# Performance work log

Hardware: AMD Instinct MI355X
Metric: run time of the kernel (lower is better)

## Reference

```python
import jax, jax.numpy as jnp
import numpy as np

DELTA_HEADING = 15.0
DELTA_BEARING = 15.0
N_HEADING = int(360 // 15)  # 24
N_BEARING = int(360 // 15)  # 24
MASK_FILL = 1e24


def setup_inputs() -> dict:
    key = jax.random.key(0)
    k1, k2, k3, k4, k5, k6 = jax.random.split(key, 6)
    N, B, H = 128, 256, 128
    hidden_state = jax.random.normal(k1, (N, B, H), dtype=jnp.float32)
    # distances in a realistic positive range
    distance_matrix = jax.random.uniform(k2, (B, N, N), dtype=jnp.float32, minval=0.0, maxval=10.0)
    bearing_matrix = jax.random.uniform(k3, (B, N, N), dtype=jnp.float32, minval=0.0, maxval=360.0)
    heading_matrix = jax.random.uniform(k4, (B, N, N), dtype=jnp.float32, minval=0.0, maxval=360.0)
    # mostly-valid sequence mask (bool, per batch x vessel)
    sequence_mask = jax.random.uniform(k5, (B, N)) > 0.1
    domain = jax.random.normal(k6, (N_HEADING, N_BEARING), dtype=jnp.float32)
    return {
        "hidden_state": hidden_state,
        "distance_matrix": distance_matrix,
        "bearing_matrix": bearing_matrix,
        "heading_matrix": heading_matrix,
        "sequence_mask": sequence_mask,
        "domain": domain,
    }


def reference(hidden_state, distance_matrix, bearing_matrix, heading_matrix, sequence_mask, domain):
    # indices into learned domain table
    idx1 = jnp.clip(jnp.floor(heading_matrix / DELTA_HEADING), 0, N_HEADING - 1).astype(jnp.int32)
    idx2 = jnp.clip(jnp.floor(bearing_matrix / DELTA_BEARING), 0, N_BEARING - 1).astype(jnp.int32)
    # pairwise validity mask: (B,N,1) & (B,1,N)
    wmask = sequence_mask[:, :, None] & sequence_mask[:, None, :]
    dist = jnp.where(wmask, distance_matrix, MASK_FILL)
    weights = jax.nn.softplus(domain[idx1, idx2] - dist)  # (B,N,N)
    # hidden_state: (N,B,H) -> (B,N,H); weighted sum over neighbors j
    h = jnp.swapaxes(hidden_state, 0, 1)
    weighted_hidden = jnp.tanh(jnp.einsum('bij,bjh->bih', weights, h))
    weighted_hidden = jnp.where(sequence_mask[:, :, None], weighted_hidden, 0.0)
    return weighted_hidden
```

## Files before the change

kernel.cpp:

```cpp
#include <hip/hip_runtime.h>

#define NV 128
#define NB 256
#define NH 128
#define KC 32
#define HSTR 136

typedef __attribute__((ext_vector_type(8))) unsigned short ushort8;
typedef __attribute__((ext_vector_type(4))) float f32x4;
typedef __attribute__((ext_vector_type(8))) __bf16 bf16x8;

__device__ __forceinline__ unsigned short f2bf(float x) {
  unsigned u = __builtin_bit_cast(unsigned, x);
  return (unsigned short)((u + 0x7fffu + ((u >> 16) & 1u)) >> 16);
}
__device__ __forceinline__ float bf2f(unsigned short h) {
  return __builtin_bit_cast(float, (unsigned)h << 16);
}

__launch_bounds__(512, 1)
__global__ void spatial_attn_mfma(const float* __restrict__ hidden,
                                  const float* __restrict__ dist,
                                  const float* __restrict__ brg,
                                  const float* __restrict__ hdg,
                                  const unsigned char* __restrict__ maskraw,
                                  const float* __restrict__ domain,
                                  float* __restrict__ out) {
  __shared__ unsigned short thi[NH * HSTR];
  __shared__ unsigned short tlo[NH * HSTR];
  __shared__ float dom[24 * 24];
  __shared__ float maskf[NV];
  __shared__ int kindsh;

  const int tid = threadIdx.x;
  const int lane = tid & 63;
  const int wv = tid >> 6;
  const int b = blockIdx.x;

  for (int k = tid; k < 576; k += 512) dom[k] = domain[k];
  if (tid == 0) kindsh = 1;
  const unsigned char s1 = maskraw[(size_t)(b & 63) * 512 + 4 * (tid & 127) + 1];
  __syncthreads();
  if (s1 != 0) kindsh = 0;
  __syncthreads();
  if (tid < NV) {
    const int m = kindsh ? ((const int*)maskraw)[b * NV + tid]
                         : (int)maskraw[b * NV + tid];
    maskf[tid] = (m != 0) ? 1.0f : 0.0f;
  }

  {
    const int shh = tid & 127;
    const int sj = (tid >> 7) * 32;
#pragma unroll
    for (int g = 0; g < 2; ++g) {
      const int jb = sj + g * 16;
      float v[16];
#pragma unroll
      for (int k = 0; k < 16; ++k)
        v[k] = hidden[((size_t)(jb + k) * NB + b) * NH + shh];
      ushort8 ph0, ph1, pl0, pl1;
#pragma unroll
      for (int k = 0; k < 8; ++k) {
        const unsigned short h = f2bf(v[k]);
        ph0[k] = h;
        pl0[k] = f2bf(v[k] - bf2f(h));
      }
#pragma unroll
      for (int k = 0; k < 8; ++k) {
        const unsigned short h = f2bf(v[8 + k]);
        ph1[k] = h;
        pl1[k] = f2bf(v[8 + k] - bf2f(h));
      }
      *(ushort8*)&thi[shh * HSTR + jb] = ph0;
      *(ushort8*)&thi[shh * HSTR + jb + 8] = ph1;
      *(ushort8*)&tlo[shh * HSTR + jb] = pl0;
      *(ushort8*)&tlo[shh * HSTR + jb + 8] = pl1;
    }
  }

  const int fm = lane & 15;
  const int j0 = (lane >> 4) * 8;
  const int arow = 16 * wv + fm;

  const float* dR = dist + ((size_t)b * NV + arow) * NV;
  const float* bR = brg + ((size_t)b * NV + arow) * NV;
  const float* gR = hdg + ((size_t)b * NV + arow) * NV;

  float4 pd0 = *(const float4*)&dR[j0];
  float4 pd1 = *(const float4*)&dR[j0 + 4];
  float4 pb0 = *(const float4*)&bR[j0];
  float4 pb1 = *(const float4*)&bR[j0 + 4];
  float4 pg0 = *(const float4*)&gR[j0];
  float4 pg1 = *(const float4*)&gR[j0 + 4];

  f32x4 acc[8];
#pragma unroll
  for (int t = 0; t < 8; ++t) acc[t] = (f32x4)0.0f;

  __syncthreads();

#pragma unroll
  for (int cs = 0; cs < 4; ++cs) {
    const int jc = cs * KC;

    const float dv[8] = {pd0.x, pd0.y, pd0.z, pd0.w, pd1.x, pd1.y, pd1.z, pd1.w};
    const float bv[8] = {pb0.x, pb0.y, pb0.z, pb0.w, pb1.x, pb1.y, pb1.z, pb1.w};
    const float gv[8] = {pg0.x, pg0.y, pg0.z, pg0.w, pg1.x, pg1.y, pg1.z, pg1.w};

    if (cs < 3) {
      const int jn = (cs + 1) * KC + j0;
      pd0 = *(const float4*)&dR[jn];
      pd1 = *(const float4*)&dR[jn + 4];
      pb0 = *(const float4*)&bR[jn];
      pb1 = *(const float4*)&bR[jn + 4];
      pg0 = *(const float4*)&gR[jn];
      pg1 = *(const float4*)&gR[jn + 4];
    }

    ushort8 ahi_u, alo_u;
#pragma unroll
    for (int e = 0; e < 8; ++e) {
      const int i1 = min(23, max(0, (int)floorf(gv[e] * (1.0f / 15.0f))));
      const int i2 = min(23, max(0, (int)floorf(bv[e] * (1.0f / 15.0f))));
      const float t = dom[i1 * 24 + i2] - dv[e];
      const float sp = fmaxf(t, 0.0f) + __logf(1.0f + __expf(-fabsf(t)));
      const float w = sp * maskf[jc + j0 + e];
      const unsigned short h = f2bf(w);
      ahi_u[e] = h;
      alo_u[e] = f2bf(w - bf2f(h));
    }
    const bf16x8 ahi = __builtin_bit_cast(bf16x8, ahi_u);
    const bf16x8 alo = __builtin_bit_cast(bf16x8, alo_u);

#pragma unroll
    for (int t = 0; t < 8; ++t) {
      const int boff = (16 * t + fm) * HSTR + jc + j0;
      const bf16x8 bhi = __builtin_bit_cast(bf16x8, *(const ushort8*)&thi[boff]);
      const bf16x8 blo = __builtin_bit_cast(bf16x8, *(const ushort8*)&tlo[boff]);
      acc[t] = __builtin_amdgcn_mfma_f32_16x16x32_bf16(ahi, bhi, acc[t], 0, 0, 0);
      acc[t] = __builtin_amdgcn_mfma_f32_16x16x32_bf16(ahi, blo, acc[t], 0, 0, 0);
      acc[t] = __builtin_amdgcn_mfma_f32_16x16x32_bf16(alo, bhi, acc[t], 0, 0, 0);
    }
  }

  float* oB = out + (size_t)b * NV * NH;
  const int rbase = 16 * wv + 4 * (lane >> 4);
#pragma unroll
  for (int t = 0; t < 8; ++t) {
    const int hh = 16 * t + fm;
#pragma unroll
    for (int r = 0; r < 4; ++r) {
      const int i = rbase + r;
      const float x = acc[t][r];
      const float ex = __expf(2.0f * x);
      const float th = 1.0f - __fdividef(2.0f, ex + 1.0f);
      oB[i * NH + hh] = th * maskf[i];
    }
  }
}

extern "C" void kernel_launch(void* const* d_in, const int* in_sizes, int n_in,
                              void* d_out, int out_size, void* d_ws, size_t ws_size,
                              hipStream_t stream) {
  const float* hidden = (const float*)d_in[0];
  const float* dist = (const float*)d_in[1];
  const float* brg = (const float*)d_in[2];
  const float* hdg = (const float*)d_in[3];
  const unsigned char* mask = (const unsigned char*)d_in[4];
  const float* domain = (const float*)d_in[5];
  float* out = (float*)d_out;

  spatial_attn_mfma<<<NB, 512, 0, stream>>>(hidden, dist, brg, hdg, mask,
                                            domain, out);
}
```

Baseline: 24.47 us.

## Issue all attention-matrix loads upfront and replace mask-detection barriers with wave vote

Issues every distance, bearing and heading load for all four K-chunks at kernel start, before the hidden-state staging, so the whole global working set is in flight at once. The hidden-state gather now loads all 32 values before converting, which deepens memory-level parallelism. The mask-format detection (byte vs int32 bool) switches from a shared-memory flag with two block barriers to a per-wave __any vote, removing two __syncthreads. The cost is much higher register pressure from holding 24 float4s plus 32 floats, which could spill at 512 threads per block.

```diff
diff --git a/kernel.cpp b/kernel.cpp
--- a/kernel.cpp
+++ b/kernel.cpp
@@ -30,54 +30,11 @@
   __shared__ unsigned short tlo[NH * HSTR];
   __shared__ float dom[24 * 24];
   __shared__ float maskf[NV];
-  __shared__ int kindsh;
 
   const int tid = threadIdx.x;
   const int lane = tid & 63;
   const int wv = tid >> 6;
   const int b = blockIdx.x;
-
-  for (int k = tid; k < 576; k += 512) dom[k] = domain[k];
-  if (tid == 0) kindsh = 1;
-  const unsigned char s1 = maskraw[(size_t)(b & 63) * 512 + 4 * (tid & 127) + 1];
-  __syncthreads();
-  if (s1 != 0) kindsh = 0;
-  __syncthreads();
-  if (tid < NV) {
-    const int m = kindsh ? ((const int*)maskraw)[b * NV + tid]
-                         : (int)maskraw[b * NV + tid];
-    maskf[tid] = (m != 0) ? 1.0f : 0.0f;
-  }
-
-  {
-    const int shh = tid & 127;
-    const int sj = (tid >> 7) * 32;
-#pragma unroll
-    for (int g = 0; g < 2; ++g) {
-      const int jb = sj + g * 16;
-      float v[16];
-#pragma unroll
-      for (int k = 0; k < 16; ++k)
-        v[k] = hidden[((size_t)(jb + k) * NB + b) * NH + shh];
-      ushort8 ph0, ph1, pl0, pl1;
-#pragma unroll
-      for (int k = 0; k < 8; ++k) {
-        const unsigned short h = f2bf(v[k]);
-        ph0[k] = h;
-        pl0[k] = f2bf(v[k] - bf2f(h));
-      }
-#pragma unroll
-      for (int k = 0; k < 8; ++k) {
-        const unsigned short h = f2bf(v[8 + k]);
-        ph1[k] = h;
-        pl1[k] = f2bf(v[8 + k] - bf2f(h));
-      }
-      *(ushort8*)&thi[shh * HSTR + jb] = ph0;
-      *(ushort8*)&thi[shh * HSTR + jb + 8] = ph1;
-      *(ushort8*)&tlo[shh * HSTR + jb] = pl0;
-      *(ushort8*)&tlo[shh * HSTR + jb + 8] = pl1;
-    }
-  }
 
   const int fm = lane & 15;
   const int j0 = (lane >> 4) * 8;
@@ -87,12 +44,52 @@
   const float* bR = brg + ((size_t)b * NV + arow) * NV;
   const float* gR = hdg + ((size_t)b * NV + arow) * NV;
 
-  float4 pd0 = *(const float4*)&dR[j0];
-  float4 pd1 = *(const float4*)&dR[j0 + 4];
-  float4 pb0 = *(const float4*)&bR[j0];
-  float4 pb1 = *(const float4*)&bR[j0 + 4];
-  float4 pg0 = *(const float4*)&gR[j0];
-  float4 pg1 = *(const float4*)&gR[j0 + 4];
+  const size_t wbase = (size_t)(b & 63) * 512;
+  const unsigned char sA = maskraw[wbase + 8 * lane + 1];
+  const unsigned char sB = maskraw[wbase + 8 * lane + 5];
+
+  float4 pd[4][2], pb[4][2], pg[4][2];
+#pragma unroll
+  for (int c = 0; c < 4; ++c) {
+    const int jn = c * KC + j0;
+    pd[c][0] = *(const float4*)&dR[jn];
+    pd[c][1] = *(const float4*)&dR[jn + 4];
+    pb[c][0] = *(const float4*)&bR[jn];
+    pb[c][1] = *(const float4*)&bR[jn + 4];
+    pg[c][0] = *(const float4*)&gR[jn];
+    pg[c][1] = *(const float4*)&gR[jn + 4];
+  }
+
+  const bool bytewise = __any((int)(sA | sB)) != 0;
+
+  if (tid < NV) {
+    const int m = bytewise ? (int)maskraw[b * NV + tid]
+                           : ((const int*)maskraw)[b * NV + tid];
+    maskf[tid] = (m != 0) ? 1.0f : 0.0f;
+  }
+
+  for (int k = tid; k < 576; k += 512) dom[k] = domain[k];
+
+  {
+    const int shh = tid & 127;
+    const int sj = (tid >> 7) * 32;
+    float v[32];
+#pragma unroll
+    for (int k = 0; k < 32; ++k)
+      v[k] = hidden[((size_t)(sj + k) * NB + b) * NH + shh];
+#pragma unroll
+    for (int g = 0; g < 4; ++g) {
+      ushort8 ph, pl;
+#pragma unroll
+      for (int k = 0; k < 8; ++k) {
+        const unsigned short h = f2bf(v[8 * g + k]);
+        ph[k] = h;
+        pl[k] = f2bf(v[8 * g + k] - bf2f(h));
+      }
+      *(ushort8*)&thi[shh * HSTR + sj + 8 * g] = ph;
+      *(ushort8*)&tlo[shh * HSTR + sj + 8 * g] = pl;
+    }
+  }
 
   f32x4 acc[8];
 #pragma unroll
@@ -103,20 +100,12 @@
 #pragma unroll
   for (int cs = 0; cs < 4; ++cs) {
     const int jc = cs * KC;
-
-    const float dv[8] = {pd0.x, pd0.y, pd0.z, pd0.w, pd1.x, pd1.y, pd1.z, pd1.w};
-    const float bv[8] = {pb0.x, pb0.y, pb0.z, pb0.w, pb1.x, pb1.y, pb1.z, pb1.w};
-    const float gv[8] = {pg0.x, pg0.y, pg0.z, pg0.w, pg1.x, pg1.y, pg1.z, pg1.w};
-
-    if (cs < 3) {
-      const int jn = (cs + 1) * KC + j0;
-      pd0 = *(const float4*)&dR[jn];
-      pd1 = *(const float4*)&dR[jn + 4];
-      pb0 = *(const float4*)&bR[jn];
-      pb1 = *(const float4*)&bR[jn + 4];
-      pg0 = *(const float4*)&gR[jn];
-      pg1 = *(const float4*)&gR[jn + 4];
-    }
+    const float dv[8] = {pd[cs][0].x, pd[cs][0].y, pd[cs][0].z, pd[cs][0].w,
+                         pd[cs][1].x, pd[cs][1].y, pd[cs][1].z, pd[cs][1].w};
+    const float bv[8] = {pb[cs][0].x, pb[cs][0].y, pb[cs][0].z, pb[cs][0].w,
+                         pb[cs][1].x, pb[cs][1].y, pb[cs][1].z, pb[cs][1].w};
+    const float gv[8] = {pg[cs][0].x, pg[cs][0].y, pg[cs][0].z, pg[cs][0].w,
+                         pg[cs][1].x, pg[cs][1].y, pg[cs][1].z, pg[cs][1].w};
 
     ushort8 ahi_u, alo_u;
 #pragma unroll
```

Measured after the change: 25.73 us. +5.2%, slower.
